# Kernel tuning notes

Hardware: AMD Instinct MI355X
Metric: run time of the kernel (lower is better)

The kernel has to match this reference:

```python
import jax, jax.numpy as jnp
import numpy as np

B, C, N, S = 4, 64, 16384, 16
DIM_OUT = 64
SCALE = DIM_OUT ** (-0.5)


def setup_inputs() -> dict:
    key = jax.random.key(0)
    ks = jax.random.split(key, 8)
    return {
        "xyz": jax.random.normal(ks[0], (B, 3, N), dtype=jnp.float32),
        "neighbor_xyz": jax.random.normal(ks[1], (B, 3, N, S), dtype=jnp.float32),
        "points": jax.random.normal(ks[2], (B, C, N), dtype=jnp.float32),
        "neighbor_points": jax.random.normal(ks[3], (B, C, N, S), dtype=jnp.float32),
        "Wk": jax.random.normal(ks[4], (C, C), dtype=jnp.float32) * 0.05,
        "Wv": jax.random.normal(ks[5], (DIM_OUT, C + 3), dtype=jnp.float32) * 0.05,
        "Wp": jax.random.normal(ks[6], (C, 4), dtype=jnp.float32) * 0.05,
        "bp": jax.random.normal(ks[7], (C,), dtype=jnp.float32) * 0.05,
    }


def reference(xyz, neighbor_xyz, points, neighbor_points, Wk, Wv, Wp, bp):
    # relative position of each neighbor: [B,3,N,S]
    tmp = xyz[:, :, :, None] - neighbor_xyz
    xyz_norm = jnp.sqrt(jnp.sum(tmp * tmp, axis=1, keepdims=True))  # [B,1,N,S]
    pos = jnp.concatenate([tmp, xyz_norm], axis=1)  # [B,4,N,S]

    # 1x1 convs == per-point channel matmuls
    pos_enc = jnp.einsum('oc,bcns->bons', Wp, pos) + bp[None, :, None, None]
    k = jnp.einsum('oc,bcns->bons', Wk, neighbor_points + pos_enc)  # [B,C,N,S]
    v_in = jnp.concatenate([neighbor_points, tmp], axis=1)  # [B,C+3,N,S]
    v = jnp.einsum('oc,bcns->bons', Wv, v_in)  # [B,dim_out,N,S]

    q = points * SCALE  # [B,C,N]
    attn = jax.nn.softmax(jnp.einsum('bcn,bcns->bns', q, k), axis=-1)  # [B,N,S]
    out = jnp.einsum('bns,bcns->bcn', attn, v)  # [B,dim_out,N]
    return out
```

## Files before the change

### kernel.cpp

```cpp
#include <hip/hip_runtime.h>
#include <math.h>

constexpr int Nn = 16384;
constexpr int ST = 68;
constexpr size_t NS = (size_t)Nn * 16;

template <int CTRL>
__device__ __forceinline__ float dpp_f(float x) {
    return __int_as_float(
        __builtin_amdgcn_update_dpp(0, __float_as_int(x), CTRL, 0xF, 0xF, false));
}
__device__ __forceinline__ float rsum16(float v) {
    v += dpp_f<0x128>(v); v += dpp_f<0x124>(v);
    v += dpp_f<0x122>(v); v += dpp_f<0x121>(v);
    return v;
}
__device__ __forceinline__ float rmax16(float v) {
    v = fmaxf(v, dpp_f<0x128>(v)); v = fmaxf(v, dpp_f<0x124>(v));
    v = fmaxf(v, dpp_f<0x122>(v)); v = fmaxf(v, dpp_f<0x121>(v));
    return v;
}

__global__ __launch_bounds__(256, 4) void qkpp_kernel(
    const float* __restrict__ points, const float* __restrict__ Wk,
    const float* __restrict__ Wp, float* __restrict__ ws)
{
    const int tid = threadIdx.x;
    const int lane = tid & 63;
    const int q = lane >> 4;
    const int pt = blockIdx.x * 64 + (tid >> 6) * 16 + (lane & 15);
    const int b = pt >> 14;
    const int n = pt & (Nn - 1);

    float qk[16];
#pragma unroll
    for (int k = 0; k < 16; ++k) qk[k] = 0.f;

    const float* prow = points + (size_t)b * 64 * Nn + n;
    const float* wkq = Wk + 16 * q;
#pragma unroll 4
    for (int c = 0; c < 64; ++c) {
        const float qv = prow[(size_t)c * Nn];
        const float4 w0 = *(const float4*)(wkq + c * 64 + 0);
        const float4 w1 = *(const float4*)(wkq + c * 64 + 4);
        const float4 w2 = *(const float4*)(wkq + c * 64 + 8);
        const float4 w3 = *(const float4*)(wkq + c * 64 + 12);
        qk[0]  = fmaf(qv, w0.x, qk[0]);  qk[1]  = fmaf(qv, w0.y, qk[1]);
        qk[2]  = fmaf(qv, w0.z, qk[2]);  qk[3]  = fmaf(qv, w0.w, qk[3]);
        qk[4]  = fmaf(qv, w1.x, qk[4]);  qk[5]  = fmaf(qv, w1.y, qk[5]);
        qk[6]  = fmaf(qv, w1.z, qk[6]);  qk[7]  = fmaf(qv, w1.w, qk[7]);
        qk[8]  = fmaf(qv, w2.x, qk[8]);  qk[9]  = fmaf(qv, w2.y, qk[9]);
        qk[10] = fmaf(qv, w2.z, qk[10]); qk[11] = fmaf(qv, w2.w, qk[11]);
        qk[12] = fmaf(qv, w3.x, qk[12]); qk[13] = fmaf(qv, w3.y, qk[13]);
        qk[14] = fmaf(qv, w3.z, qk[14]); qk[15] = fmaf(qv, w3.w, qk[15]);
    }
#pragma unroll
    for (int k = 0; k < 16; ++k) qk[k] *= 0.125f;

    float p0 = 0.f, p1 = 0.f, p2 = 0.f, p3 = 0.f;
#pragma unroll
    for (int k = 0; k < 16; ++k) {
        const float4 wp4 = *(const float4*)(Wp + (16 * q + k) * 4);
        p0 = fmaf(qk[k], wp4.x, p0);
        p1 = fmaf(qk[k], wp4.y, p1);
        p2 = fmaf(qk[k], wp4.z, p2);
        p3 = fmaf(qk[k], wp4.w, p3);
    }
    p0 += __shfl_xor(p0, 16); p0 += __shfl_xor(p0, 32);
    p1 += __shfl_xor(p1, 16); p1 += __shfl_xor(p1, 32);
    p2 += __shfl_xor(p2, 16); p2 += __shfl_xor(p2, 32);
    p3 += __shfl_xor(p3, 16); p3 += __shfl_xor(p3, 32);

    float* orow = ws + (size_t)pt * ST + 16 * q;
    ((float4*)orow)[0] = make_float4(qk[0],  qk[1],  qk[2],  qk[3]);
    ((float4*)orow)[1] = make_float4(qk[4],  qk[5],  qk[6],  qk[7]);
    ((float4*)orow)[2] = make_float4(qk[8],  qk[9],  qk[10], qk[11]);
    ((float4*)orow)[3] = make_float4(qk[12], qk[13], qk[14], qk[15]);
    if (q == 0)
        *(float4*)(ws + (size_t)pt * ST + 64) = make_float4(p0, p1, p2, p3);
}

__global__ __launch_bounds__(256, 4) void attn_out_kernel(
    const float* __restrict__ xyz, const float* __restrict__ nxyz,
    const float* __restrict__ npts, const float* __restrict__ Wv,
    const float* __restrict__ ws, float* __restrict__ out)
{
    __shared__ float wvT[67 * 68];

    const int tid = threadIdx.x;
    for (int idx = tid; idx < 64 * 67; idx += 256) {
        const int o = idx / 67, c = idx - o * 67;
        wvT[c * 68 + o] = Wv[idx];
    }
    __syncthreads();

    const int lane = tid & 63;
    const int s = lane & 15;
    const int nn = lane >> 4;
    const int gpt = blockIdx.x * 16 + (tid >> 6) * 4;
    const int b = gpt >> 14;
    const int ng = gpt & (Nn - 1);
    const int pt = gpt + nn;

    const float* npb = npts + (size_t)(b * 64) * NS + (size_t)ng * 16 + lane;

    float npv[64];
#pragma unroll
    for (int c = 0; c < 64; ++c) npv[c] = npb[(size_t)c * NS];

    const float nx0 = nxyz[((size_t)(b * 3 + 0) * Nn + ng) * 16 + lane];
    const float nx1 = nxyz[((size_t)(b * 3 + 1) * Nn + ng) * 16 + lane];
    const float nx2 = nxyz[((size_t)(b * 3 + 2) * Nn + ng) * 16 + lane];
    const float x0 = xyz[(size_t)(b * 3 + 0) * Nn + ng + nn];
    const float x1 = xyz[(size_t)(b * 3 + 1) * Nn + ng + nn];
    const float x2 = xyz[(size_t)(b * 3 + 2) * Nn + ng + nn];
    const float d0 = x0 - nx0, d1 = x1 - nx1, d2 = x2 - nx2;
    const float dn = sqrtf(d0 * d0 + d1 * d1 + d2 * d2);

    const float* qrow = ws + (size_t)pt * ST;

    float l0 = 0.f, l1 = 0.f, l2 = 0.f, l3 = 0.f;
#pragma unroll
    for (int jc = 0; jc < 16; ++jc) {
        const float4 qq = *(const float4*)(qrow + 4 * jc);
        l0 = fmaf(qq.x, npv[4 * jc + 0], l0);
        l1 = fmaf(qq.y, npv[4 * jc + 1], l1);
        l2 = fmaf(qq.z, npv[4 * jc + 2], l2);
        l3 = fmaf(qq.w, npv[4 * jc + 3], l3);
    }
    const float4 ppv = *(const float4*)(qrow + 64);
    float logit = (l0 + l1) + (l2 + l3);
    logit += ppv.x * d0 + ppv.y * d1 + ppv.z * d2 + ppv.w * dn;

    const float mx = rmax16(logit);
    const float e = __expf(logit - mx);
    const float se = rsum16(e);
    const float attn = e / se;

    float a0 = 0.f, a1 = 0.f, a2 = 0.f, a3 = 0.f;
#pragma unroll
    for (int c = 0; c < 64; ++c) {
        const float r = rsum16(attn * npv[c]);
        const float4 wq = *(const float4*)&wvT[c * 68 + 4 * s];
        a0 = fmaf(r, wq.x, a0);
        a1 = fmaf(r, wq.y, a1);
        a2 = fmaf(r, wq.z, a2);
        a3 = fmaf(r, wq.w, a3);
    }
    {
        const float t0 = rsum16(attn * d0);
        const float t1 = rsum16(attn * d1);
        const float t2 = rsum16(attn * d2);
        const float4 wA = *(const float4*)&wvT[64 * 68 + 4 * s];
        const float4 wB = *(const float4*)&wvT[65 * 68 + 4 * s];
        const float4 wC = *(const float4*)&wvT[66 * 68 + 4 * s];
        a0 = fmaf(t0, wA.x, a0); a1 = fmaf(t0, wA.y, a1);
        a2 = fmaf(t0, wA.z, a2); a3 = fmaf(t0, wA.w, a3);
        a0 = fmaf(t1, wB.x, a0); a1 = fmaf(t1, wB.y, a1);
        a2 = fmaf(t1, wB.z, a2); a3 = fmaf(t1, wB.w, a3);
        a0 = fmaf(t2, wC.x, a0); a1 = fmaf(t2, wC.y, a1);
        a2 = fmaf(t2, wC.z, a2); a3 = fmaf(t2, wC.w, a3);
    }

    float* ob = out + ((size_t)(b * 64 + 4 * s) * Nn) + ng + nn;
    ob[0]          = a0;
    ob[(size_t)Nn]     = a1;
    ob[(size_t)Nn * 2] = a2;
    ob[(size_t)Nn * 3] = a3;
}

extern "C" void kernel_launch(void* const* d_in, const int* in_sizes, int n_in,
                              void* d_out, int out_size, void* d_ws, size_t ws_size,
                              hipStream_t stream) {
    const float* xyz    = (const float*)d_in[0];
    const float* nxyz   = (const float*)d_in[1];
    const float* points = (const float*)d_in[2];
    const float* npts   = (const float*)d_in[3];
    const float* Wk     = (const float*)d_in[4];
    const float* Wv     = (const float*)d_in[5];
    const float* Wp     = (const float*)d_in[6];
    float* out = (float*)d_out;
    float* ws = (float*)d_ws;

    hipLaunchKernelGGL(qkpp_kernel,     dim3(1024), dim3(256), 0, stream,
                       points, Wk, Wp, ws);
    hipLaunchKernelGGL(attn_out_kernel, dim3(4096), dim3(256), 0, stream,
                       xyz, nxyz, npts, Wv, ws, out);
}
```

Measured before the change: 118.1 us.

## Split attention channels across wave pairs to cut registers and raise occupancy

Each point group is now handled by two wavefronts, each holding 32 of the 64 neighbor-feature channels instead of all 64. The partial logits and partial outputs are combined through shared memory, and the grid is doubled. The launch bound rises to 6 blocks per CU. The aim is to lower register pressure so more waves are resident to hide the large memory stream. In exchange it adds two block barriers, an LDS exchange, and duplicated softmax and reduction work, and half the waves sit idle during the store.

```diff
diff --git a/kernel.cpp b/kernel.cpp
--- a/kernel.cpp
+++ b/kernel.cpp
@@ -80,12 +80,14 @@
         *(float4*)(ws + (size_t)pt * ST + 64) = make_float4(p0, p1, p2, p3);
 }
 
-__global__ __launch_bounds__(256, 4) void attn_out_kernel(
+__global__ __launch_bounds__(256, 6) void attn_out_kernel(
     const float* __restrict__ xyz, const float* __restrict__ nxyz,
     const float* __restrict__ npts, const float* __restrict__ Wv,
     const float* __restrict__ ws, float* __restrict__ out)
 {
     __shared__ float wvT[67 * 68];
+    __shared__ float lexch[4][64];
+    __shared__ float aexch[2][4][64];
 
     const int tid = threadIdx.x;
     for (int idx = tid; idx < 64 * 67; idx += 256) {
@@ -94,43 +96,52 @@
     }
     __syncthreads();
 
+    const int w = tid >> 6;
     const int lane = tid & 63;
     const int s = lane & 15;
     const int nn = lane >> 4;
-    const int gpt = blockIdx.x * 16 + (tid >> 6) * 4;
+    const int pair = w >> 1;
+    const int half = w & 1;
+    const int gpt = blockIdx.x * 8 + pair * 4;
     const int b = gpt >> 14;
     const int ng = gpt & (Nn - 1);
     const int pt = gpt + nn;
 
-    const float* npb = npts + (size_t)(b * 64) * NS + (size_t)ng * 16 + lane;
-
-    float npv[64];
-#pragma unroll
-    for (int c = 0; c < 64; ++c) npv[c] = npb[(size_t)c * NS];
-
-    const float nx0 = nxyz[((size_t)(b * 3 + 0) * Nn + ng) * 16 + lane];
-    const float nx1 = nxyz[((size_t)(b * 3 + 1) * Nn + ng) * 16 + lane];
-    const float nx2 = nxyz[((size_t)(b * 3 + 2) * Nn + ng) * 16 + lane];
-    const float x0 = xyz[(size_t)(b * 3 + 0) * Nn + ng + nn];
-    const float x1 = xyz[(size_t)(b * 3 + 1) * Nn + ng + nn];
-    const float x2 = xyz[(size_t)(b * 3 + 2) * Nn + ng + nn];
-    const float d0 = x0 - nx0, d1 = x1 - nx1, d2 = x2 - nx2;
-    const float dn = sqrtf(d0 * d0 + d1 * d1 + d2 * d2);
-
-    const float* qrow = ws + (size_t)pt * ST;
-
+    const float* npb = npts + (size_t)(b * 64 + half * 32) * NS + (size_t)ng * 16 + lane;
+    float npv[32];
+#pragma unroll
+    for (int c = 0; c < 32; ++c) npv[c] = npb[(size_t)c * NS];
+
+    float d0 = 0.f, d1 = 0.f, d2 = 0.f, dn = 0.f;
+    if (half) {
+        const float nx0 = nxyz[((size_t)(b * 3 + 0) * Nn + ng) * 16 + lane];
+        const float nx1 = nxyz[((size_t)(b * 3 + 1) * Nn + ng) * 16 + lane];
+        const float nx2 = nxyz[((size_t)(b * 3 + 2) * Nn + ng) * 16 + lane];
+        d0 = xyz[(size_t)(b * 3 + 0) * Nn + ng + nn] - nx0;
+        d1 = xyz[(size_t)(b * 3 + 1) * Nn + ng + nn] - nx1;
+        d2 = xyz[(size_t)(b * 3 + 2) * Nn + ng + nn] - nx2;
+        dn = sqrtf(d0 * d0 + d1 * d1 + d2 * d2);
+    }
+
+    const float* qrow = ws + (size_t)pt * ST + half * 32;
     float l0 = 0.f, l1 = 0.f, l2 = 0.f, l3 = 0.f;
 #pragma unroll
-    for (int jc = 0; jc < 16; ++jc) {
+    for (int jc = 0; jc < 8; ++jc) {
         const float4 qq = *(const float4*)(qrow + 4 * jc);
         l0 = fmaf(qq.x, npv[4 * jc + 0], l0);
         l1 = fmaf(qq.y, npv[4 * jc + 1], l1);
         l2 = fmaf(qq.z, npv[4 * jc + 2], l2);
         l3 = fmaf(qq.w, npv[4 * jc + 3], l3);
     }
-    const float4 ppv = *(const float4*)(qrow + 64);
-    float logit = (l0 + l1) + (l2 + l3);
-    logit += ppv.x * d0 + ppv.y * d1 + ppv.z * d2 + ppv.w * dn;
+    float lp = (l0 + l1) + (l2 + l3);
+    if (half) {
+        const float4 ppv = *(const float4*)(ws + (size_t)pt * ST + 64);
+        lp += ppv.x * d0 + ppv.y * d1 + ppv.z * d2 + ppv.w * dn;
+    }
+
+    lexch[w][lane] = lp;
+    __syncthreads();
+    const float logit = lp + lexch[w ^ 1][lane];
 
     const float mx = rmax16(logit);
     const float e = __expf(logit - mx);
@@ -139,15 +150,15 @@
 
     float a0 = 0.f, a1 = 0.f, a2 = 0.f, a3 = 0.f;
 #pragma unroll
-    for (int c = 0; c < 64; ++c) {
+    for (int c = 0; c < 32; ++c) {
         const float r = rsum16(attn * npv[c]);
-        const float4 wq = *(const float4*)&wvT[c * 68 + 4 * s];
+        const float4 wq = *(const float4*)&wvT[(half * 32 + c) * 68 + 4 * s];
         a0 = fmaf(r, wq.x, a0);
         a1 = fmaf(r, wq.y, a1);
         a2 = fmaf(r, wq.z, a2);
         a3 = fmaf(r, wq.w, a3);
     }
-    {
+    if (half) {
         const float t0 = rsum16(attn * d0);
         const float t1 = rsum16(attn * d1);
         const float t2 = rsum16(attn * d2);
@@ -160,13 +171,24 @@
         a2 = fmaf(t1, wB.z, a2); a3 = fmaf(t1, wB.w, a3);
         a0 = fmaf(t2, wC.x, a0); a1 = fmaf(t2, wC.y, a1);
         a2 = fmaf(t2, wC.z, a2); a3 = fmaf(t2, wC.w, a3);
-    }
-
-    float* ob = out + ((size_t)(b * 64 + 4 * s) * Nn) + ng + nn;
-    ob[0]          = a0;
-    ob[(size_t)Nn]     = a1;
-    ob[(size_t)Nn * 2] = a2;
-    ob[(size_t)Nn * 3] = a3;
+        aexch[pair][0][lane] = a0;
+        aexch[pair][1][lane] = a1;
+        aexch[pair][2][lane] = a2;
+        aexch[pair][3][lane] = a3;
+    }
+    __syncthreads();
+
+    if (!half) {
+        a0 += aexch[pair][0][lane];
+        a1 += aexch[pair][1][lane];
+        a2 += aexch[pair][2][lane];
+        a3 += aexch[pair][3][lane];
+        float* ob = out + ((size_t)(b * 64 + 4 * s) * Nn) + ng + nn;
+        ob[0]              = a0;
+        ob[(size_t)Nn]     = a1;
+        ob[(size_t)Nn * 2] = a2;
+        ob[(size_t)Nn * 3] = a3;
+    }
 }
 
 extern "C" void kernel_launch(void* const* d_in, const int* in_sizes, int n_in,
@@ -184,6 +206,6 @@
 
     hipLaunchKernelGGL(qkpp_kernel,     dim3(1024), dim3(256), 0, stream,
                        points, Wk, Wp, ws);
-    hipLaunchKernelGGL(attn_out_kernel, dim3(4096), dim3(256), 0, stream,
+    hipLaunchKernelGGL(attn_out_kernel, dim3(8192), dim3(256), 0, stream,
                        xyz, nxyz, npts, Wv, ws, out);
 }
```

Measured after the change: 121.2 us. +2.6%, slower.

## Split attn_out channels across waves with float4 neighbor loads and LDS reduction

Applied to the files above, without the earlier changes.

Restructures attn_out_kernel so each wave handles 16 channels for all 16 points in the block, and each lane holds 4 neighbors as float4 loads. Partial logits are reduced across waves through shared memory. Softmax and the attention-weighted sum use 4-lane DPP reductions instead of 16-lane ones. The weighted value vectors are staged in LDS and then multiplied by Wv, with each thread producing 4 output channels for one point. The intent is to cut the 64-register-per-lane scalar loads and the many 16-lane DPP reductions per channel. The cost is extra barriers, shared-memory traffic, and some imbalance because only the last wave handles xyz.

```diff
diff --git a/kernel.cpp b/kernel.cpp
--- a/kernel.cpp
+++ b/kernel.cpp
@@ -10,14 +10,14 @@
     return __int_as_float(
         __builtin_amdgcn_update_dpp(0, __float_as_int(x), CTRL, 0xF, 0xF, false));
 }
-__device__ __forceinline__ float rsum16(float v) {
-    v += dpp_f<0x128>(v); v += dpp_f<0x124>(v);
-    v += dpp_f<0x122>(v); v += dpp_f<0x121>(v);
+__device__ __forceinline__ float qsum4(float v) {
+    v += dpp_f<0xB1>(v);
+    v += dpp_f<0x4E>(v);
     return v;
 }
-__device__ __forceinline__ float rmax16(float v) {
-    v = fmaxf(v, dpp_f<0x128>(v)); v = fmaxf(v, dpp_f<0x124>(v));
-    v = fmaxf(v, dpp_f<0x122>(v)); v = fmaxf(v, dpp_f<0x121>(v));
+__device__ __forceinline__ float qmax4(float v) {
+    v = fmaxf(v, dpp_f<0xB1>(v));
+    v = fmaxf(v, dpp_f<0x4E>(v));
     return v;
 }
 
@@ -86,87 +86,121 @@
     const float* __restrict__ ws, float* __restrict__ out)
 {
     __shared__ float wvT[67 * 68];
+    __shared__ __align__(16) float lexch[4][64][4];
+    __shared__ float vbexch[67 * 17];
 
     const int tid = threadIdx.x;
+    const int w = tid >> 6;
+    const int l = tid & 63;
+    const int p = l >> 2;
+    const int sq = l & 3;
+    const int gpt0 = blockIdx.x * 16;
+    const int b = gpt0 >> 14;
+    const int ng = gpt0 & (Nn - 1);
+
+    const float* npb = npts + ((size_t)(b * 64 + 16 * w)) * NS + (size_t)ng * 16 + 4 * l;
+    float4 npv4[16];
+#pragma unroll
+    for (int k = 0; k < 16; ++k) npv4[k] = *(const float4*)(npb + (size_t)k * NS);
+
+    const float* qrow = ws + (size_t)(gpt0 + p) * ST + 16 * w;
+    const float4 qqa = ((const float4*)qrow)[0];
+    const float4 qqb = ((const float4*)qrow)[1];
+    const float4 qqc = ((const float4*)qrow)[2];
+    const float4 qqd = ((const float4*)qrow)[3];
+
+    float4 d04, d14, d24, dn4, pp4;
+    if (w == 3) {
+        const float4 nx0 = *(const float4*)(nxyz + ((size_t)(b * 3 + 0) * Nn + ng) * 16 + 4 * l);
+        const float4 nx1 = *(const float4*)(nxyz + ((size_t)(b * 3 + 1) * Nn + ng) * 16 + 4 * l);
+        const float4 nx2 = *(const float4*)(nxyz + ((size_t)(b * 3 + 2) * Nn + ng) * 16 + 4 * l);
+        const float x0 = xyz[(size_t)(b * 3 + 0) * Nn + ng + p];
+        const float x1 = xyz[(size_t)(b * 3 + 1) * Nn + ng + p];
+        const float x2 = xyz[(size_t)(b * 3 + 2) * Nn + ng + p];
+        d04 = make_float4(x0 - nx0.x, x0 - nx0.y, x0 - nx0.z, x0 - nx0.w);
+        d14 = make_float4(x1 - nx1.x, x1 - nx1.y, x1 - nx1.z, x1 - nx1.w);
+        d24 = make_float4(x2 - nx2.x, x2 - nx2.y, x2 - nx2.z, x2 - nx2.w);
+        dn4 = make_float4(sqrtf(d04.x * d04.x + d14.x * d14.x + d24.x * d24.x),
+                          sqrtf(d04.y * d04.y + d14.y * d14.y + d24.y * d24.y),
+                          sqrtf(d04.z * d04.z + d14.z * d14.z + d24.z * d24.z),
+                          sqrtf(d04.w * d04.w + d14.w * d14.w + d24.w * d24.w));
+        pp4 = *(const float4*)(ws + (size_t)(gpt0 + p) * ST + 64);
+    }
+
     for (int idx = tid; idx < 64 * 67; idx += 256) {
         const int o = idx / 67, c = idx - o * 67;
         wvT[c * 68 + o] = Wv[idx];
     }
+
+    const float qks[16] = {qqa.x, qqa.y, qqa.z, qqa.w, qqb.x, qqb.y, qqb.z, qqb.w,
+                           qqc.x, qqc.y, qqc.z, qqc.w, qqd.x, qqd.y, qqd.z, qqd.w};
+    float4 lp = make_float4(0.f, 0.f, 0.f, 0.f);
+#pragma unroll
+    for (int k = 0; k < 16; ++k) {
+        lp.x = fmaf(qks[k], npv4[k].x, lp.x);
+        lp.y = fmaf(qks[k], npv4[k].y, lp.y);
+        lp.z = fmaf(qks[k], npv4[k].z, lp.z);
+        lp.w = fmaf(qks[k], npv4[k].w, lp.w);
+    }
+    if (w == 3) {
+        lp.x += pp4.x * d04.x + pp4.y * d14.x + pp4.z * d24.x + pp4.w * dn4.x;
+        lp.y += pp4.x * d04.y + pp4.y * d14.y + pp4.z * d24.y + pp4.w * dn4.y;
+        lp.z += pp4.x * d04.z + pp4.y * d14.z + pp4.z * d24.z + pp4.w * dn4.z;
+        lp.w += pp4.x * d04.w + pp4.y * d14.w + pp4.z * d24.w + pp4.w * dn4.w;
+    }
+
     __syncthreads();
-
-    const int lane = tid & 63;
-    const int s = lane & 15;
-    const int nn = lane >> 4;
-    const int gpt = blockIdx.x * 16 + (tid >> 6) * 4;
-    const int b = gpt >> 14;
-    const int ng = gpt & (Nn - 1);
-    const int pt = gpt + nn;
-
-    const float* npb = npts + (size_t)(b * 64) * NS + (size_t)ng * 16 + lane;
-
-    float npv[64];
-#pragma unroll
-    for (int c = 0; c < 64; ++c) npv[c] = npb[(size_t)c * NS];
-
-    const float nx0 = nxyz[((size_t)(b * 3 + 0) * Nn + ng) * 16 + lane];
-    const float nx1 = nxyz[((size_t)(b * 3 + 1) * Nn + ng) * 16 + lane];
-    const float nx2 = nxyz[((size_t)(b * 3 + 2) * Nn + ng) * 16 + lane];
-    const float x0 = xyz[(size_t)(b * 3 + 0) * Nn + ng + nn];
-    const float x1 = xyz[(size_t)(b * 3 + 1) * Nn + ng + nn];
-    const float x2 = xyz[(size_t)(b * 3 + 2) * Nn + ng + nn];
-    const float d0 = x0 - nx0, d1 = x1 - nx1, d2 = x2 - nx2;
-    const float dn = sqrtf(d0 * d0 + d1 * d1 + d2 * d2);
-
-    const float* qrow = ws + (size_t)pt * ST;
-
-    float l0 = 0.f, l1 = 0.f, l2 = 0.f, l3 = 0.f;
-#pragma unroll
-    for (int jc = 0; jc < 16; ++jc) {
-        const float4 qq = *(const float4*)(qrow + 4 * jc);
-        l0 = fmaf(qq.x, npv[4 * jc + 0], l0);
-        l1 = fmaf(qq.y, npv[4 * jc + 1], l1);
-        l2 = fmaf(qq.z, npv[4 * jc + 2], l2);
-        l3 = fmaf(qq.w, npv[4 * jc + 3], l3);
-    }
-    const float4 ppv = *(const float4*)(qrow + 64);
-    float logit = (l0 + l1) + (l2 + l3);
-    logit += ppv.x * d0 + ppv.y * d1 + ppv.z * d2 + ppv.w * dn;
-
-    const float mx = rmax16(logit);
-    const float e = __expf(logit - mx);
-    const float se = rsum16(e);
-    const float attn = e / se;
-
-    float a0 = 0.f, a1 = 0.f, a2 = 0.f, a3 = 0.f;
-#pragma unroll
-    for (int c = 0; c < 64; ++c) {
-        const float r = rsum16(attn * npv[c]);
-        const float4 wq = *(const float4*)&wvT[c * 68 + 4 * s];
-        a0 = fmaf(r, wq.x, a0);
-        a1 = fmaf(r, wq.y, a1);
-        a2 = fmaf(r, wq.z, a2);
-        a3 = fmaf(r, wq.w, a3);
-    }
-    {
-        const float t0 = rsum16(attn * d0);
-        const float t1 = rsum16(attn * d1);
-        const float t2 = rsum16(attn * d2);
-        const float4 wA = *(const float4*)&wvT[64 * 68 + 4 * s];
-        const float4 wB = *(const float4*)&wvT[65 * 68 + 4 * s];
-        const float4 wC = *(const float4*)&wvT[66 * 68 + 4 * s];
-        a0 = fmaf(t0, wA.x, a0); a1 = fmaf(t0, wA.y, a1);
-        a2 = fmaf(t0, wA.z, a2); a3 = fmaf(t0, wA.w, a3);
-        a0 = fmaf(t1, wB.x, a0); a1 = fmaf(t1, wB.y, a1);
-        a2 = fmaf(t1, wB.z, a2); a3 = fmaf(t1, wB.w, a3);
-        a0 = fmaf(t2, wC.x, a0); a1 = fmaf(t2, wC.y, a1);
-        a2 = fmaf(t2, wC.z, a2); a3 = fmaf(t2, wC.w, a3);
-    }
-
-    float* ob = out + ((size_t)(b * 64 + 4 * s) * Nn) + ng + nn;
-    ob[0]          = a0;
-    ob[(size_t)Nn]     = a1;
-    ob[(size_t)Nn * 2] = a2;
-    ob[(size_t)Nn * 3] = a3;
+    *(float4*)&lexch[w][l][0] = lp;
+    __syncthreads();
+    const float4 g0 = *(const float4*)&lexch[0][l][0];
+    const float4 g1 = *(const float4*)&lexch[1][l][0];
+    const float4 g2 = *(const float4*)&lexch[2][l][0];
+    const float4 g3 = *(const float4*)&lexch[3][l][0];
+    const float4 lg = make_float4(g0.x + g1.x + g2.x + g3.x,
+                                  g0.y + g1.y + g2.y + g3.y,
+                                  g0.z + g1.z + g2.z + g3.z,
+                                  g0.w + g1.w + g2.w + g3.w);
+
+    float mx = fmaxf(fmaxf(lg.x, lg.y), fmaxf(lg.z, lg.w));
+    mx = qmax4(mx);
+    const float e0 = __expf(lg.x - mx), e1 = __expf(lg.y - mx);
+    const float e2 = __expf(lg.z - mx), e3 = __expf(lg.w - mx);
+    const float se = qsum4((e0 + e1) + (e2 + e3));
+    const float inv = 1.0f / se;
+    const float at0 = e0 * inv, at1 = e1 * inv, at2 = e2 * inv, at3 = e3 * inv;
+
+#pragma unroll
+    for (int k = 0; k < 16; ++k) {
+        float v = at0 * npv4[k].x + at1 * npv4[k].y + at2 * npv4[k].z + at3 * npv4[k].w;
+        v = qsum4(v);
+        if (sq == (k & 3)) vbexch[(16 * w + k) * 17 + p] = v;
+    }
+    if (w == 3) {
+        const float t0 = qsum4(at0 * d04.x + at1 * d04.y + at2 * d04.z + at3 * d04.w);
+        const float t1 = qsum4(at0 * d14.x + at1 * d14.y + at2 * d14.z + at3 * d14.w);
+        const float t2 = qsum4(at0 * d24.x + at1 * d24.y + at2 * d24.z + at3 * d24.w);
+        if (sq == 0) vbexch[64 * 17 + p] = t0;
+        else if (sq == 1) vbexch[65 * 17 + p] = t1;
+        else if (sq == 2) vbexch[66 * 17 + p] = t2;
+    }
+    __syncthreads();
+
+    float4 oa = make_float4(0.f, 0.f, 0.f, 0.f);
+#pragma unroll
+    for (int c = 0; c < 67; ++c) {
+        const float vb = vbexch[c * 17 + p];
+        const float4 wq = *(const float4*)&wvT[c * 68 + 16 * w + 4 * sq];
+        oa.x = fmaf(vb, wq.x, oa.x);
+        oa.y = fmaf(vb, wq.y, oa.y);
+        oa.z = fmaf(vb, wq.z, oa.z);
+        oa.w = fmaf(vb, wq.w, oa.w);
+    }
+
+    float* ob = out + ((size_t)(b * 64 + 16 * w + 4 * sq)) * Nn + ng + p;
+    ob[0]              = oa.x;
+    ob[(size_t)Nn]     = oa.y;
+    ob[(size_t)Nn * 2] = oa.z;
+    ob[(size_t)Nn * 3] = oa.w;
 }
 
 extern "C" void kernel_launch(void* const* d_in, const int* in_sizes, int n_in,
```

New measurement: 117.9 us. No clear change (-0.2%).

## Fuse query-key projection into attention kernel with LDS and prefetch loop

Applied to the files above, without the earlier changes.

Merges the two kernels into one. Each block computes Wk-projected queries and position projections for its 64 points into LDS rather than a global workspace. Each wave then loops over four 4-point groups, prefetching the next group's neighbor features and coordinates into registers while it reduces the current group. This removes the workspace write and read and one launch, and overlaps loads with compute. In exchange the grid is four times smaller and the kernel uses more LDS, which can reduce parallelism.

```diff
diff --git a/kernel.cpp b/kernel.cpp
--- a/kernel.cpp
+++ b/kernel.cpp
@@ -2,8 +2,8 @@
 #include <math.h>
 
 constexpr int Nn = 16384;
-constexpr int ST = 68;
 constexpr size_t NS = (size_t)Nn * 16;
+constexpr int GPW = 4;
 
 template <int CTRL>
 __device__ __forceinline__ float dpp_f(float x) {
@@ -21,152 +21,166 @@
     return v;
 }
 
-__global__ __launch_bounds__(256, 4) void qkpp_kernel(
-    const float* __restrict__ points, const float* __restrict__ Wk,
-    const float* __restrict__ Wp, float* __restrict__ ws)
-{
-    const int tid = threadIdx.x;
-    const int lane = tid & 63;
-    const int q = lane >> 4;
-    const int pt = blockIdx.x * 64 + (tid >> 6) * 16 + (lane & 15);
-    const int b = pt >> 14;
-    const int n = pt & (Nn - 1);
-
-    float qk[16];
-#pragma unroll
-    for (int k = 0; k < 16; ++k) qk[k] = 0.f;
-
-    const float* prow = points + (size_t)b * 64 * Nn + n;
-    const float* wkq = Wk + 16 * q;
-#pragma unroll 4
-    for (int c = 0; c < 64; ++c) {
-        const float qv = prow[(size_t)c * Nn];
-        const float4 w0 = *(const float4*)(wkq + c * 64 + 0);
-        const float4 w1 = *(const float4*)(wkq + c * 64 + 4);
-        const float4 w2 = *(const float4*)(wkq + c * 64 + 8);
-        const float4 w3 = *(const float4*)(wkq + c * 64 + 12);
-        qk[0]  = fmaf(qv, w0.x, qk[0]);  qk[1]  = fmaf(qv, w0.y, qk[1]);
-        qk[2]  = fmaf(qv, w0.z, qk[2]);  qk[3]  = fmaf(qv, w0.w, qk[3]);
-        qk[4]  = fmaf(qv, w1.x, qk[4]);  qk[5]  = fmaf(qv, w1.y, qk[5]);
-        qk[6]  = fmaf(qv, w1.z, qk[6]);  qk[7]  = fmaf(qv, w1.w, qk[7]);
-        qk[8]  = fmaf(qv, w2.x, qk[8]);  qk[9]  = fmaf(qv, w2.y, qk[9]);
-        qk[10] = fmaf(qv, w2.z, qk[10]); qk[11] = fmaf(qv, w2.w, qk[11]);
-        qk[12] = fmaf(qv, w3.x, qk[12]); qk[13] = fmaf(qv, w3.y, qk[13]);
-        qk[14] = fmaf(qv, w3.z, qk[14]); qk[15] = fmaf(qv, w3.w, qk[15]);
-    }
-#pragma unroll
-    for (int k = 0; k < 16; ++k) qk[k] *= 0.125f;
-
-    float p0 = 0.f, p1 = 0.f, p2 = 0.f, p3 = 0.f;
-#pragma unroll
-    for (int k = 0; k < 16; ++k) {
-        const float4 wp4 = *(const float4*)(Wp + (16 * q + k) * 4);
-        p0 = fmaf(qk[k], wp4.x, p0);
-        p1 = fmaf(qk[k], wp4.y, p1);
-        p2 = fmaf(qk[k], wp4.z, p2);
-        p3 = fmaf(qk[k], wp4.w, p3);
-    }
-    p0 += __shfl_xor(p0, 16); p0 += __shfl_xor(p0, 32);
-    p1 += __shfl_xor(p1, 16); p1 += __shfl_xor(p1, 32);
-    p2 += __shfl_xor(p2, 16); p2 += __shfl_xor(p2, 32);
-    p3 += __shfl_xor(p3, 16); p3 += __shfl_xor(p3, 32);
-
-    float* orow = ws + (size_t)pt * ST + 16 * q;
-    ((float4*)orow)[0] = make_float4(qk[0],  qk[1],  qk[2],  qk[3]);
-    ((float4*)orow)[1] = make_float4(qk[4],  qk[5],  qk[6],  qk[7]);
-    ((float4*)orow)[2] = make_float4(qk[8],  qk[9],  qk[10], qk[11]);
-    ((float4*)orow)[3] = make_float4(qk[12], qk[13], qk[14], qk[15]);
-    if (q == 0)
-        *(float4*)(ws + (size_t)pt * ST + 64) = make_float4(p0, p1, p2, p3);
-}
-
-__global__ __launch_bounds__(256, 4) void attn_out_kernel(
+#define BAR() do { asm volatile("s_waitcnt lgkmcnt(0)" ::: "memory"); \
+    __builtin_amdgcn_s_barrier(); asm volatile("" ::: "memory"); } while (0)
+
+__global__ __launch_bounds__(256, 4) void attn_fused_kernel(
     const float* __restrict__ xyz, const float* __restrict__ nxyz,
-    const float* __restrict__ npts, const float* __restrict__ Wv,
-    const float* __restrict__ ws, float* __restrict__ out)
+    const float* __restrict__ points, const float* __restrict__ npts,
+    const float* __restrict__ Wk, const float* __restrict__ Wv,
+    const float* __restrict__ Wp, float* __restrict__ out)
 {
     __shared__ float wvT[67 * 68];
+    __shared__ float qk_lds[64 * 68];
 
     const int tid = threadIdx.x;
+    const int w = tid >> 6;
+    const int l = tid & 63;
+    const int s = l & 15;
+    const int nn = l >> 4;
+    const int gptbase = blockIdx.x * 64;
+    const int b = gptbase >> 14;
+    const int ngbase = gptbase & (Nn - 1);
+    const int nw = ngbase + w * 16;
+
     for (int idx = tid; idx < 64 * 67; idx += 256) {
         const int o = idx / 67, c = idx - o * 67;
         wvT[c * 68 + o] = Wv[idx];
     }
-    __syncthreads();
-
-    const int lane = tid & 63;
-    const int s = lane & 15;
-    const int nn = lane >> 4;
-    const int gpt = blockIdx.x * 16 + (tid >> 6) * 4;
-    const int b = gpt >> 14;
-    const int ng = gpt & (Nn - 1);
-    const int pt = gpt + nn;
-
-    const float* npb = npts + (size_t)(b * 64) * NS + (size_t)ng * 16 + lane;
-
+
+    const float* npb0 = npts + (size_t)(b * 64) * NS + (size_t)nw * 16 + l;
     float npv[64];
 #pragma unroll
-    for (int c = 0; c < 64; ++c) npv[c] = npb[(size_t)c * NS];
-
-    const float nx0 = nxyz[((size_t)(b * 3 + 0) * Nn + ng) * 16 + lane];
-    const float nx1 = nxyz[((size_t)(b * 3 + 1) * Nn + ng) * 16 + lane];
-    const float nx2 = nxyz[((size_t)(b * 3 + 2) * Nn + ng) * 16 + lane];
-    const float x0 = xyz[(size_t)(b * 3 + 0) * Nn + ng + nn];
-    const float x1 = xyz[(size_t)(b * 3 + 1) * Nn + ng + nn];
-    const float x2 = xyz[(size_t)(b * 3 + 2) * Nn + ng + nn];
-    const float d0 = x0 - nx0, d1 = x1 - nx1, d2 = x2 - nx2;
-    const float dn = sqrtf(d0 * d0 + d1 * d1 + d2 * d2);
-
-    const float* qrow = ws + (size_t)pt * ST;
-
-    float l0 = 0.f, l1 = 0.f, l2 = 0.f, l3 = 0.f;
-#pragma unroll
-    for (int jc = 0; jc < 16; ++jc) {
-        const float4 qq = *(const float4*)(qrow + 4 * jc);
-        l0 = fmaf(qq.x, npv[4 * jc + 0], l0);
-        l1 = fmaf(qq.y, npv[4 * jc + 1], l1);
-        l2 = fmaf(qq.z, npv[4 * jc + 2], l2);
-        l3 = fmaf(qq.w, npv[4 * jc + 3], l3);
+    for (int c = 0; c < 64; ++c) npv[c] = npb0[(size_t)c * NS];
+    float nxa = nxyz[((size_t)(b * 3 + 0) * Nn + nw) * 16 + l];
+    float nxb = nxyz[((size_t)(b * 3 + 1) * Nn + nw) * 16 + l];
+    float nxc = nxyz[((size_t)(b * 3 + 2) * Nn + nw) * 16 + l];
+    float xa = xyz[(size_t)(b * 3 + 0) * Nn + nw + nn];
+    float xb = xyz[(size_t)(b * 3 + 1) * Nn + nw + nn];
+    float xc = xyz[(size_t)(b * 3 + 2) * Nn + nw + nn];
+
+    {
+        const int quarter = l >> 4;
+        const int ptl = w * 16 + (l & 15);
+        const int n = ngbase + ptl;
+
+        float qk[16];
+#pragma unroll
+        for (int k = 0; k < 16; ++k) qk[k] = 0.f;
+
+        const float* prow = points + (size_t)b * 64 * Nn + n;
+        const float* wkq = Wk + 16 * quarter;
+#pragma unroll 4
+        for (int c = 0; c < 64; ++c) {
+            const float qv = prow[(size_t)c * Nn];
+            const float4 w0 = *(const float4*)(wkq + c * 64 + 0);
+            const float4 w1 = *(const float4*)(wkq + c * 64 + 4);
+            const float4 w2 = *(const float4*)(wkq + c * 64 + 8);
+            const float4 w3 = *(const float4*)(wkq + c * 64 + 12);
+            qk[0]  = fmaf(qv, w0.x, qk[0]);  qk[1]  = fmaf(qv, w0.y, qk[1]);
+            qk[2]  = fmaf(qv, w0.z, qk[2]);  qk[3]  = fmaf(qv, w0.w, qk[3]);
+            qk[4]  = fmaf(qv, w1.x, qk[4]);  qk[5]  = fmaf(qv, w1.y, qk[5]);
+            qk[6]  = fmaf(qv, w1.z, qk[6]);  qk[7]  = fmaf(qv, w1.w, qk[7]);
+            qk[8]  = fmaf(qv, w2.x, qk[8]);  qk[9]  = fmaf(qv, w2.y, qk[9]);
+            qk[10] = fmaf(qv, w2.z, qk[10]); qk[11] = fmaf(qv, w2.w, qk[11]);
+            qk[12] = fmaf(qv, w3.x, qk[12]); qk[13] = fmaf(qv, w3.y, qk[13]);
+            qk[14] = fmaf(qv, w3.z, qk[14]); qk[15] = fmaf(qv, w3.w, qk[15]);
+        }
+#pragma unroll
+        for (int k = 0; k < 16; ++k) qk[k] *= 0.125f;
+
+        float p0 = 0.f, p1 = 0.f, p2 = 0.f, p3 = 0.f;
+#pragma unroll
+        for (int k = 0; k < 16; ++k) {
+            const float4 wp4 = *(const float4*)(Wp + (16 * quarter + k) * 4);
+            p0 = fmaf(qk[k], wp4.x, p0);
+            p1 = fmaf(qk[k], wp4.y, p1);
+            p2 = fmaf(qk[k], wp4.z, p2);
+            p3 = fmaf(qk[k], wp4.w, p3);
+        }
+        p0 += __shfl_xor(p0, 16); p0 += __shfl_xor(p0, 32);
+        p1 += __shfl_xor(p1, 16); p1 += __shfl_xor(p1, 32);
+        p2 += __shfl_xor(p2, 16); p2 += __shfl_xor(p2, 32);
+        p3 += __shfl_xor(p3, 16); p3 += __shfl_xor(p3, 32);
+
+        float* orow = qk_lds + ptl * 68 + 16 * quarter;
+        ((float4*)orow)[0] = make_float4(qk[0],  qk[1],  qk[2],  qk[3]);
+        ((float4*)orow)[1] = make_float4(qk[4],  qk[5],  qk[6],  qk[7]);
+        ((float4*)orow)[2] = make_float4(qk[8],  qk[9],  qk[10], qk[11]);
+        ((float4*)orow)[3] = make_float4(qk[12], qk[13], qk[14], qk[15]);
+        if (quarter == 0)
+            *(float4*)(qk_lds + ptl * 68 + 64) = make_float4(p0, p1, p2, p3);
     }
-    const float4 ppv = *(const float4*)(qrow + 64);
-    float logit = (l0 + l1) + (l2 + l3);
-    logit += ppv.x * d0 + ppv.y * d1 + ppv.z * d2 + ppv.w * dn;
-
-    const float mx = rmax16(logit);
-    const float e = __expf(logit - mx);
-    const float se = rsum16(e);
-    const float attn = e / se;
-
-    float a0 = 0.f, a1 = 0.f, a2 = 0.f, a3 = 0.f;
-#pragma unroll
-    for (int c = 0; c < 64; ++c) {
-        const float r = rsum16(attn * npv[c]);
-        const float4 wq = *(const float4*)&wvT[c * 68 + 4 * s];
-        a0 = fmaf(r, wq.x, a0);
-        a1 = fmaf(r, wq.y, a1);
-        a2 = fmaf(r, wq.z, a2);
-        a3 = fmaf(r, wq.w, a3);
+    BAR();
+
+#pragma unroll 1
+    for (int g = 0; g < GPW; ++g) {
+        const int ng = nw + 4 * g;
+
+        const float d0 = xa - nxa, d1 = xb - nxb, d2 = xc - nxc;
+        const float dn = sqrtf(d0 * d0 + d1 * d1 + d2 * d2);
+
+        {
+            const int gn = (g + 1 < GPW) ? g + 1 : g;
+            const size_t go = (size_t)gn * 64;
+            nxa = nxyz[((size_t)(b * 3 + 0) * Nn + nw) * 16 + go + l];
+            nxb = nxyz[((size_t)(b * 3 + 1) * Nn + nw) * 16 + go + l];
+            nxc = nxyz[((size_t)(b * 3 + 2) * Nn + nw) * 16 + go + l];
+            xa = xyz[(size_t)(b * 3 + 0) * Nn + nw + 4 * gn + nn];
+            xb = xyz[(size_t)(b * 3 + 1) * Nn + nw + 4 * gn + nn];
+            xc = xyz[(size_t)(b * 3 + 2) * Nn + nw + 4 * gn + nn];
+        }
+
+        const float* qrow = qk_lds + (w * 16 + 4 * g + nn) * 68;
+        float l0 = 0.f, l1 = 0.f, l2 = 0.f, l3 = 0.f;
+#pragma unroll
+        for (int j = 0; j < 16; ++j) {
+            const float4 qv = ((const float4*)qrow)[j];
+            l0 = fmaf(qv.x, npv[4 * j + 0], l0);
+            l1 = fmaf(qv.y, npv[4 * j + 1], l1);
+            l2 = fmaf(qv.z, npv[4 * j + 2], l2);
+            l3 = fmaf(qv.w, npv[4 * j + 3], l3);
+        }
+        const float4 pp = ((const float4*)qrow)[16];
+        float logit = (l0 + l1) + (l2 + l3);
+        logit += pp.x * d0 + pp.y * d1 + pp.z * d2 + pp.w * dn;
+
+        const float mx = rmax16(logit);
+        const float e = __expf(logit - mx);
+        const float se = rsum16(e);
+        const float attn = e / se;
+
+        const float* npb_n = npb0 + (size_t)((g + 1 < GPW) ? g + 1 : g) * 64;
+        float4 oa = make_float4(0.f, 0.f, 0.f, 0.f);
+#pragma unroll
+        for (int c = 0; c < 64; ++c) {
+            const float r = rsum16(attn * npv[c]);
+            const float4 wq = *(const float4*)&wvT[c * 68 + 4 * s];
+            oa.x = fmaf(r, wq.x, oa.x);
+            oa.y = fmaf(r, wq.y, oa.y);
+            oa.z = fmaf(r, wq.z, oa.z);
+            oa.w = fmaf(r, wq.w, oa.w);
+            npv[c] = npb_n[(size_t)c * NS];
+        }
+        {
+            const float t0 = rsum16(attn * d0);
+            const float t1 = rsum16(attn * d1);
+            const float t2 = rsum16(attn * d2);
+            const float4 wA = *(const float4*)&wvT[64 * 68 + 4 * s];
+            const float4 wB = *(const float4*)&wvT[65 * 68 + 4 * s];
+            const float4 wC = *(const float4*)&wvT[66 * 68 + 4 * s];
+            oa.x += t0 * wA.x + t1 * wB.x + t2 * wC.x;
+            oa.y += t0 * wA.y + t1 * wB.y + t2 * wC.y;
+            oa.z += t0 * wA.z + t1 * wB.z + t2 * wC.z;
+            oa.w += t0 * wA.w + t1 * wB.w + t2 * wC.w;
+        }
+
+        float* ob = out + ((size_t)(b * 64 + 4 * s)) * Nn + ng + nn;
+        ob[0]              = oa.x;
+        ob[(size_t)Nn]     = oa.y;
+        ob[(size_t)Nn * 2] = oa.z;
+        ob[(size_t)Nn * 3] = oa.w;
     }
-    {
-        const float t0 = rsum16(attn * d0);
-        const float t1 = rsum16(attn * d1);
-        const float t2 = rsum16(attn * d2);
-        const float4 wA = *(const float4*)&wvT[64 * 68 + 4 * s];
-        const float4 wB = *(const float4*)&wvT[65 * 68 + 4 * s];
-        const float4 wC = *(const float4*)&wvT[66 * 68 + 4 * s];
-        a0 = fmaf(t0, wA.x, a0); a1 = fmaf(t0, wA.y, a1);
-        a2 = fmaf(t0, wA.z, a2); a3 = fmaf(t0, wA.w, a3);
-        a0 = fmaf(t1, wB.x, a0); a1 = fmaf(t1, wB.y, a1);
-        a2 = fmaf(t1, wB.z, a2); a3 = fmaf(t1, wB.w, a3);
-        a0 = fmaf(t2, wC.x, a0); a1 = fmaf(t2, wC.y, a1);
-        a2 = fmaf(t2, wC.z, a2); a3 = fmaf(t2, wC.w, a3);
-    }
-
-    float* ob = out + ((size_t)(b * 64 + 4 * s) * Nn) + ng + nn;
-    ob[0]          = a0;
-    ob[(size_t)Nn]     = a1;
-    ob[(size_t)Nn * 2] = a2;
-    ob[(size_t)Nn * 3] = a3;
 }
 
 extern "C" void kernel_launch(void* const* d_in, const int* in_sizes, int n_in,
@@ -180,10 +194,7 @@
     const float* Wv     = (const float*)d_in[5];
     const float* Wp     = (const float*)d_in[6];
     float* out = (float*)d_out;
-    float* ws = (float*)d_ws;
-
-    hipLaunchKernelGGL(qkpp_kernel,     dim3(1024), dim3(256), 0, stream,
-                       points, Wk, Wp, ws);
-    hipLaunchKernelGGL(attn_out_kernel, dim3(4096), dim3(256), 0, stream,
-                       xyz, nxyz, npts, Wv, ws, out);
-}
+
+    hipLaunchKernelGGL(attn_fused_kernel, dim3(1024), dim3(256), 0, stream,
+                       xyz, nxyz, points, npts, Wk, Wv, Wp, out);
+}
```

New measurement: 373.4 us. 3.16x slower.
